# Performance work log

Measured on AMD Instinct MI355X. Metric: run time of the kernel, lower is better.

## Reference

```python
import jax, jax.numpy as jnp
import numpy as np
import math

DIM = 1024
N_HEADS = 16
HEAD_DIM = DIM // N_HEADS
MAX_SEQ_LEN = 2048


def rope_tables(seq_len, head_dim):
    inv_freq = 1.0 / (10000.0 ** (jnp.arange(0, head_dim, 2, dtype=jnp.float32) / head_dim))
    t = jnp.arange(seq_len, dtype=jnp.float32)
    freqs = jnp.einsum('i,j->ij', t, inv_freq)          # [T, D/2]
    emb = jnp.concatenate([freqs, freqs], axis=-1)      # [T, D]
    return jnp.cos(emb), jnp.sin(emb)


def rotate_half(x):
    x1, x2 = jnp.split(x, 2, axis=-1)
    return jnp.concatenate([-x2, x1], axis=-1)


def setup_inputs() -> dict:
    key = jax.random.key(0)
    k1, k2, k3 = jax.random.split(key, 3)
    B, T = 4, 2048
    x = jax.random.normal(k1, (B, T, DIM), dtype=jnp.float32)
    # Linear(dim, 3*dim, bias=False) and Linear(dim, dim, bias=False); stored as [in, out]
    Wqkv = jax.random.normal(k2, (DIM, 3 * DIM), dtype=jnp.float32) * (1.0 / math.sqrt(DIM))
    Wproj = jax.random.normal(k3, (DIM, DIM), dtype=jnp.float32) * (1.0 / math.sqrt(DIM))
    return {"x": x, "Wqkv": Wqkv, "Wproj": Wproj}


def reference(x, Wqkv, Wproj):
    B, T, C = x.shape
    qkv = x @ Wqkv                                       # [B,T,3C]
    q, k, v = jnp.split(qkv, 3, axis=-1)
    # [B,T,C] -> [B,H,T,D]
    def to_heads(t_):
        return t_.reshape(B, T, N_HEADS, HEAD_DIM).transpose(0, 2, 1, 3)
    q, k, v = to_heads(q), to_heads(k), to_heads(v)
    cos, sin = rope_tables(T, HEAD_DIM)                  # [T,D]
    cos = cos[None, None, :, :]
    sin = sin[None, None, :, :]
    q = q * cos + rotate_half(q) * sin
    k = k * cos + rotate_half(k) * sin
    scale = 1.0 / math.sqrt(HEAD_DIM)
    att = jnp.einsum('bhqd,bhkd->bhqk', q, k) * scale    # [B,H,T,T]
    causal = jnp.triu(jnp.ones((T, T), dtype=bool), k=1)
    att = jnp.where(causal[None, None], -jnp.inf, att)
    att = jax.nn.softmax(att, axis=-1)
    y = jnp.einsum('bhqk,bhkd->bhqd', att, v)            # [B,H,T,D]
    y = y.transpose(0, 2, 1, 3).reshape(B, T, C)
    return y @ Wproj
```

## Files before the change

### kernel.cpp

```cpp
#include <hip/hip_runtime.h>
#include <hip/hip_bf16.h>

typedef unsigned short u16;
typedef __attribute__((ext_vector_type(8))) short short8;
typedef __attribute__((ext_vector_type(4))) float floatx4;

__device__ __forceinline__ u16 f2bf(float f) {
    union { float f; unsigned u; } v; v.f = f;
    unsigned r = v.u + 0x7fffu + ((v.u >> 16) & 1u);
    return (u16)(r >> 16);
}
__device__ __forceinline__ float fexp2(float x) {
#if __has_builtin(__builtin_amdgcn_exp2f)
    return __builtin_amdgcn_exp2f(x);
#else
    return exp2f(x);
#endif
}
__device__ __forceinline__ unsigned cvtpk_bf16(float lo, float hi) {
    unsigned r;
    asm("v_cvt_pk_bf16_f32 %0, %1, %2" : "=v"(r) : "v"(lo), "v"(hi));
    return r;
}
__device__ __forceinline__ void permlane32_swap(unsigned &a, unsigned &b) {
    asm("v_permlane32_swap_b32 %0, %1" : "+v"(a), "+v"(b));
}
__device__ __forceinline__ void permlane16_swap(unsigned &a, unsigned &b) {
    asm("v_permlane16_swap_b32 %0, %1" : "+v"(a), "+v"(b));
}

__device__ __forceinline__ void async_load16(const void* g, void* l) {
    __builtin_amdgcn_global_load_lds(
        (const __attribute__((address_space(1))) unsigned int*)g,
        (__attribute__((address_space(3))) unsigned int*)l, 16, 0, 0);
}

#define B_   4
#define T_   2048
#define NH_  16
#define HD_  64
#define DIM_ 1024
#define M_   (B_ * T_)
#define NQKV (3 * DIM_)
#define NT_  16
#define LOG2E 1.4426950408889634f

__global__ void cvt_x(const float* __restrict__ in, u16* __restrict__ out) {
    int idx = blockIdx.x * 256 + threadIdx.x;
    float4 v = ((const float4*)in)[idx];
    ushort4 o;
    o.x = f2bf(v.x); o.y = f2bf(v.y); o.z = f2bf(v.z); o.w = f2bf(v.w);
    ((ushort4*)out)[idx] = o;
}

__global__ void transpose_cvt(const float* __restrict__ in, u16* __restrict__ out,
                              int R, int Cn) {
    __shared__ float tile[32][33];
    int c0 = blockIdx.x * 32, r0 = blockIdx.y * 32;
    int tx = threadIdx.x, ty = threadIdx.y;
#pragma unroll
    for (int i = 0; i < 4; ++i)
        tile[ty + i * 8][tx] = in[(size_t)(r0 + ty + i * 8) * Cn + c0 + tx];
    __syncthreads();
#pragma unroll
    for (int i = 0; i < 4; ++i)
        out[(size_t)(c0 + ty + i * 8) * R + r0 + tx] = f2bf(tile[tx][ty + i * 8]);
}

__global__ void rope_table(float* __restrict__ tabc, float* __restrict__ tabs) {
    int idx = blockIdx.x * 256 + threadIdx.x;
    if (idx >= T_ * 32) return;
    int t = idx >> 5, j = idx & 31;
    double invf = pow(10000.0, -(double)j / 32.0);
    double th = (double)t * invf;
    tabc[idx] = (float)cos(th);
    tabs[idx] = (float)sin(th);
}

__global__ void v_transpose(const u16* __restrict__ Vh, u16* __restrict__ Vt) {
    __shared__ u16 tile[64 * 68];
    const int tid = threadIdx.x;
    const int bh = blockIdx.y, b = bh >> 4, h = bh & 15;
    const int t0 = blockIdx.x * 64;
    {
        int lr = tid >> 2;
        int lc = tid & 3;
        const u16* src = Vh + ((size_t)(b * T_ + t0 + lr)) * DIM_ + h * HD_;
#pragma unroll
        for (int j = 0; j < 4; ++j) {
            int c = (lc + j * 4) * 4;
            *(uint2*)&tile[lr * 68 + c] = *(const uint2*)(src + c);
        }
    }
    __syncthreads();
    {
        int d2 = tid >> 3, tseg = tid & 7;
        u16 lo8[8], hi8[8];
#pragma unroll
        for (int j = 0; j < 8; ++j) {
            unsigned w = *(const unsigned*)&tile[(tseg * 8 + j) * 68 + d2 * 2];
            lo8[j] = (u16)(w & 0xffffu);
            hi8[j] = (u16)(w >> 16);
        }
        size_t ob = ((size_t)bh * HD_ + 2 * d2) * T_ + t0 + tseg * 8;
        *(uint4*)(Vt + ob) = *(const uint4*)lo8;
        *(uint4*)(Vt + ob + T_) = *(const uint4*)hi8;
    }
}

__device__ __forceinline__ void gemm_core(const u16* __restrict__ A,
                                          const u16* __restrict__ Bt,
                                          u16* smem, int m0, int n0, int tid,
                                          floatx4 (&acc)[4][4]) {
    const int wave = tid >> 6, lane = tid & 63;
    const int ln15 = lane & 15, quad = lane >> 4;
    const int wm = (wave & 1) * 64, wn = (wave >> 1) * 64;
    const int l8 = lane & 7, ld8 = lane >> 3;
    const int sgc = (l8 ^ ld8) * 8;
    const int K = DIM_;

    const u16* aS = A + (size_t)(m0 + wave * 16 + ld8) * K + sgc;
    const u16* bS = Bt + (size_t)(n0 + wave * 32 + ld8) * K + sgc;

    auto issueA_B0 = [&](int k2, u16* As2, u16* Bs2) {
        async_load16(aS + k2,          As2 + (wave * 16) * 64);
        async_load16(aS + 8 * K + k2,  As2 + (wave * 16 + 8) * 64);
        async_load16(bS + k2,          Bs2 + (wave * 32) * 64);
    };
    auto issueB123 = [&](int k2, u16* Bs2) {
        async_load16(bS + 8 * K + k2,  Bs2 + (wave * 32 + 8) * 64);
        async_load16(bS + 16 * K + k2, Bs2 + (wave * 32 + 16) * 64);
        async_load16(bS + 24 * K + k2, Bs2 + (wave * 32 + 24) * 64);
    };
    auto compute = [&](const u16* As_c, const u16* Bs_c, int c4) {
        short8 af[4], bfv[4];
#pragma unroll
        for (int i = 0; i < 4; ++i) {
            int row = wm + i * 16 + ln15;
            af[i] = *(const short8*)&As_c[row * 64 + (((c4 + quad) ^ (row & 7)) << 3)];
        }
#pragma unroll
        for (int j = 0; j < 4; ++j) {
            int row = wn + j * 16 + ln15;
            bfv[j] = *(const short8*)&Bs_c[row * 64 + (((c4 + quad) ^ (row & 7)) << 3)];
        }
        __builtin_amdgcn_s_setprio(1);
#pragma unroll
        for (int i = 0; i < 4; ++i)
#pragma unroll
            for (int j = 0; j < 4; ++j)
                acc[i][j] = __builtin_amdgcn_mfma_f32_16x16x32_bf16(
                    af[i], bfv[j], acc[i][j], 0, 0, 0);
        __builtin_amdgcn_s_setprio(0);
    };

    issueA_B0(0, smem, smem + 24576);
    issueB123(0, smem + 24576);
    issueA_B0(64, smem + 8192, smem + 24576 + 16384);
    issueB123(64, smem + 24576 + 16384);

#pragma unroll 1
    for (int t = 0; t < NT_; ++t) {
        if (t < NT_ - 1) asm volatile("s_waitcnt vmcnt(6)" ::: "memory");
        else             asm volatile("s_waitcnt vmcnt(0)" ::: "memory");
        __builtin_amdgcn_s_barrier();
        asm volatile("" ::: "memory");

        const int cb = t % 3, cb2 = (t + 2) % 3;
        const u16* As_c = smem + cb * 8192;
        const u16* Bs_c = smem + 24576 + cb * 16384;
        u16* As2 = smem + cb2 * 8192;
        u16* Bs2 = smem + 24576 + cb2 * 16384;
        const bool iss = t < NT_ - 2;
        const int k2 = (t + 2) * 64;

        if (iss) issueA_B0(k2, As2, Bs2);
        compute(As_c, Bs_c, 0);
        asm volatile("" ::: "memory");
        __builtin_amdgcn_s_barrier();
        asm volatile("" ::: "memory");

        if (iss) issueB123(k2, Bs2);
        compute(As_c, Bs_c, 4);
        asm volatile("" ::: "memory");
    }
}

__global__ __launch_bounds__(512, 2) void gemm_qkv(const u16* __restrict__ A,
                                                   const u16* __restrict__ Bt,
                                                   const float* __restrict__ tabc,
                                                   const float* __restrict__ tabs,
                                                   u16* __restrict__ Qo,
                                                   u16* __restrict__ Ko,
                                                   u16* __restrict__ Vh) {
    __shared__ __align__(16) u16 smem[73728];
    const int tid = threadIdx.x;
    const int bid = blockIdx.x;
    const int wg = (bid & 7) * 96 + (bid >> 3);
    const int bx = wg / 64, by = wg - bx * 64;
    const int m0 = by * 128, n0 = bx * 256;

    floatx4 acc[4][4] = {};
    gemm_core(A, Bt, smem, m0, n0, tid, acc);

    const int wave = tid >> 6, lane = tid & 63;
    const int ln15 = lane & 15, quad = lane >> 4;
    const int wm = (wave & 1) * 64, wn = (wave >> 1) * 64;

    __syncthreads();
    u16* Es = smem;
    const int sel = n0 >> 10;
    auto es_put = [&](int row, int col, u16 v) {
        int c = col >> 3;
        int pc = (c & 24) | ((c & 7) ^ (row & 7));
        Es[row * 256 + pc * 8 + (col & 7)] = v;
    };
    if (sel == 2) {
#pragma unroll
        for (int i = 0; i < 4; ++i)
#pragma unroll
            for (int j = 0; j < 4; ++j)
#pragma unroll
                for (int r = 0; r < 4; ++r)
                    es_put(wm + i * 16 + quad * 4 + r, wn + j * 16 + ln15,
                           f2bf(acc[i][j][r]));
    } else {
        const float scale = sel ? 1.0f : 0.125f * LOG2E;
#pragma unroll
        for (int i = 0; i < 4; ++i)
#pragma unroll
            for (int jjl = 0; jjl < 2; ++jjl) {
                int j = jjl * 16 + ln15;
#pragma unroll
                for (int r = 0; r < 4; ++r) {
                    int row = wm + i * 16 + quad * 4 + r;
                    int t = (m0 + row) & (T_ - 1);
                    float cs = tabc[t * 32 + j], sn = tabs[t * 32 + j];
                    float xl = acc[i][jjl][r], xh = acc[i][jjl + 2][r];
                    es_put(row, wn + j,      f2bf((xl * cs - xh * sn) * scale));
                    es_put(row, wn + j + 32, f2bf((xh * cs + xl * sn) * scale));
                }
            }
    }
    __syncthreads();
    const int bb = m0 >> 11;
    u16* outqk = (sel == 1) ? Ko : Qo;
#pragma unroll
    for (int k = 0; k < 8; ++k) {
        int cid = tid + k * 512;
        int row = cid >> 5, c = cid & 31;
        int pc = (c & 24) | ((c & 7) ^ (row & 7));
        uint4 v = *(const uint4*)&Es[row * 256 + pc * 8];
        if (sel == 2) {
            *(uint4*)&Vh[(size_t)(m0 + row) * DIM_ + (n0 & 1023) + c * 8] = v;
        } else {
            int h = ((n0 & 1023) >> 6) + (c >> 3);
            int d = (c & 7) * 8;
            int t = (m0 + row) & (T_ - 1);
            *(uint4*)&outqk[((size_t)(bb * NH_ + h) * T_ + t) * HD_ + d] = v;
        }
    }
}

__global__ __launch_bounds__(512, 2) void gemm_proj(const u16* __restrict__ A,
                                                    const u16* __restrict__ Bt,
                                                    float* __restrict__ C) {
    __shared__ __align__(16) u16 smem[73728];
    const int tid = threadIdx.x;
    const int bid = blockIdx.x;
    const int wg = (bid & 7) * 32 + (bid >> 3);
    const int bx = wg / 64, by = wg - bx * 64;
    const int m0 = by * 128, n0 = bx * 256;

    floatx4 acc[4][4] = {};
    gemm_core(A, Bt, smem, m0, n0, tid, acc);

    const int wave = tid >> 6, lane = tid & 63;
    const int ln15 = lane & 15, quad = lane >> 4;
    const int wm = (wave & 1) * 64, wn = (wave >> 1) * 64;
#pragma unroll
    for (int i = 0; i < 4; ++i)
#pragma unroll
        for (int j = 0; j < 4; ++j)
#pragma unroll
            for (int r = 0; r < 4; ++r) {
                int m = m0 + wm + i * 16 + quad * 4 + r;
                int n = n0 + wn + j * 16 + ln15;
                C[(size_t)m * DIM_ + n] = acc[i][j][r];
            }
}

__global__ __launch_bounds__(256, 5) void attn_kernel(const u16* __restrict__ Q,
                                                      const u16* __restrict__ Kh,
                                                      const u16* __restrict__ Vt,
                                                      u16* __restrict__ Y) {
    __shared__ __align__(16) u16 Kl[2][64 * 64];
    __shared__ __align__(16) u16 Vl[2][64 * 64];
    const int tid = threadIdx.x, wave = tid >> 6, lane = tid & 63;
    const int ln15 = lane & 15, quad = lane >> 4;
    const int bid = blockIdx.x;
    const int wg = (bid & 7) * 128 + (bid >> 3);
    const int p = wg & 15;
    const int bh = wg >> 4;
    const int b = bh >> 4, h = bh & 15;
    const int l8 = lane & 7, ld8 = lane >> 3;
    const int sgc = l8 ^ ld8;

    const u16* kbase = Kh + (size_t)bh * T_ * HD_;
    const u16* vbase = Vt + (size_t)bh * HD_ * T_;
    const short8 ones = {0x3F80, 0x3F80, 0x3F80, 0x3F80,
                         0x3F80, 0x3F80, 0x3F80, 0x3F80};
    const int srow = wave * 16;

#pragma unroll
    for (int half = 0; half < 2; ++half) {
        const int tidx = half ? p : (31 - p);
        const int q0 = tidx * 64;
        const int bm = q0 + srow;

        const u16* qp = Q + ((size_t)bh * T_ + bm + ln15) * HD_;
        short8 qf0 = *(const short8*)(qp + quad * 8);
        short8 qf1 = *(const short8*)(qp + 32 + quad * 8);

        floatx4 o[5] = {};

        __syncthreads();
#pragma unroll
        for (int it = 0; it < 2; ++it) {
            int r = srow + it * 8;
            async_load16(kbase + (size_t)(r + ld8) * HD_ + sgc * 8, &Kl[0][r * 64]);
            async_load16(vbase + (size_t)(r + ld8) * T_ + sgc * 8, &Vl[0][r * 64]);
        }

        for (int kt = 0; kt <= tidx; ++kt) {
            const int cur = kt & 1;
            __syncthreads();
            if (kt < tidx) {
                const int kn = (kt + 1) * 64;
#pragma unroll
                for (int it = 0; it < 2; ++it) {
                    int r = srow + it * 8;
                    async_load16(kbase + (size_t)(kn + r + ld8) * HD_ + sgc * 8,
                                 &Kl[cur ^ 1][r * 64]);
                    async_load16(vbase + (size_t)(r + ld8) * T_ + kn + sgc * 8,
                                 &Vl[cur ^ 1][r * 64]);
                }
            }
            floatx4 s[4] = {};
            __builtin_amdgcn_s_setprio(1);
#pragma unroll
            for (int nt = 0; nt < 4; ++nt) {
                int row = nt * 16 + ln15;
                short8 kf0 = *(const short8*)&Kl[cur][row * 64 + ((quad ^ (row & 7)) << 3)];
                short8 kf1 = *(const short8*)&Kl[cur][row * 64 + (((4 + quad) ^ (row & 7)) << 3)];
                s[nt] = __builtin_amdgcn_mfma_f32_16x16x32_bf16(kf0, qf0, s[nt], 0, 0, 0);
                s[nt] = __builtin_amdgcn_mfma_f32_16x16x32_bf16(kf1, qf1, s[nt], 0, 0, 0);
            }
            __builtin_amdgcn_s_setprio(0);
            if (kt == tidx) {
                const int lim = srow + ln15;
#pragma unroll
                for (int nt = 0; nt < 4; ++nt) {
                    int key = nt * 16 + quad * 4;
#pragma unroll
                    for (int r = 0; r < 4; ++r)
                        s[nt][r] = (key + r > lim) ? 0.f : fexp2(s[nt][r]);
                }
            } else {
#pragma unroll
                for (int nt = 0; nt < 4; ++nt)
#pragma unroll
                    for (int r = 0; r < 4; ++r) s[nt][r] = fexp2(s[nt][r]);
            }
            unsigned x0 = cvtpk_bf16(s[0][0], s[0][1]);
            unsigned x1 = cvtpk_bf16(s[1][0], s[1][1]);
            unsigned y0 = cvtpk_bf16(s[0][2], s[0][3]);
            unsigned y1 = cvtpk_bf16(s[1][2], s[1][3]);
            unsigned x2 = cvtpk_bf16(s[2][0], s[2][1]);
            unsigned x3 = cvtpk_bf16(s[3][0], s[3][1]);
            unsigned y2 = cvtpk_bf16(s[2][2], s[2][3]);
            unsigned y3 = cvtpk_bf16(s[3][2], s[3][3]);
            permlane32_swap(x0, x1); permlane16_swap(x0, x1);
            permlane32_swap(y0, y1); permlane16_swap(y0, y1);
            permlane32_swap(x2, x3); permlane16_swap(x2, x3);
            permlane32_swap(y2, y3); permlane16_swap(y2, y3);
            union { unsigned u[4]; short8 s8; } pk0, pk1;
            pk0.u[0] = x0; pk0.u[1] = y0; pk0.u[2] = x1; pk0.u[3] = y1;
            pk1.u[0] = x2; pk1.u[1] = y2; pk1.u[2] = x3; pk1.u[3] = y3;
            __builtin_amdgcn_s_setprio(1);
#pragma unroll
            for (int nt = 0; nt < 4; ++nt) {
                int row = nt * 16 + ln15;
                short8 vf0 = *(const short8*)&Vl[cur][row * 64 + ((quad ^ (row & 7)) << 3)];
                short8 vf1 = *(const short8*)&Vl[cur][row * 64 + (((4 + quad) ^ (row & 7)) << 3)];
                o[nt] = __builtin_amdgcn_mfma_f32_16x16x32_bf16(pk0.s8, vf0, o[nt], 0, 0, 0);
                o[nt] = __builtin_amdgcn_mfma_f32_16x16x32_bf16(pk1.s8, vf1, o[nt], 0, 0, 0);
            }
            o[4] = __builtin_amdgcn_mfma_f32_16x16x32_bf16(pk0.s8, ones, o[4], 0, 0, 0);
            o[4] = __builtin_amdgcn_mfma_f32_16x16x32_bf16(pk1.s8, ones, o[4], 0, 0, 0);
            __builtin_amdgcn_s_setprio(0);
        }
#pragma unroll
        for (int r = 0; r < 4; ++r) {
            float inv = 1.f / o[4][r];
            int row = bm + quad * 4 + r;
            u16* yp = Y + ((size_t)(b * T_ + row)) * DIM_ + h * HD_;
#pragma unroll
            for (int nt = 0; nt < 4; ++nt)
                yp[nt * 16 + ln15] = f2bf(o[nt][r] * inv);
        }
    }
}

extern "C" void kernel_launch(void* const* d_in, const int* in_sizes, int n_in,
                              void* d_out, int out_size, void* d_ws, size_t ws_size,
                              hipStream_t stream) {
    const float* x     = (const float*)d_in[0];
    const float* Wqkv  = (const float*)d_in[1];
    const float* Wproj = (const float*)d_in[2];
    float* out = (float*)d_out;
    char* ws = (char*)d_ws;

    const size_t SZ_XB  = (size_t)M_ * DIM_ * 2;
    const size_t SZ_WQT = (size_t)NQKV * DIM_ * 2;
    const size_t SZ_WPT = (size_t)DIM_ * DIM_ * 2;
    const size_t SZ_Q   = SZ_XB;
    const size_t SZ_TAB = (size_t)T_ * 32 * 4;

    u16*   xb   = (u16*)(ws);
    u16*   wqt  = (u16*)(ws + SZ_XB);
    u16*   wpt  = (u16*)(ws + SZ_XB + SZ_WQT);
    u16*   qb   = (u16*)(ws + SZ_XB + SZ_WQT + SZ_WPT);
    u16*   kb   = (u16*)(ws + SZ_XB + SZ_WQT + SZ_WPT + SZ_Q);
    u16*   vhb  = (u16*)(ws + SZ_XB + SZ_WQT + SZ_WPT + 2 * SZ_Q);
    u16*   vtb  = (u16*)(ws + SZ_XB + SZ_WQT + SZ_WPT + 3 * SZ_Q);
    float* tabc = (float*)(ws + SZ_XB + SZ_WQT + SZ_WPT + 4 * SZ_Q);
    float* tabs = (float*)(ws + SZ_XB + SZ_WQT + SZ_WPT + 4 * SZ_Q + SZ_TAB);
    u16*   yb   = xb;

    rope_table<<<(T_ * 32 + 255) / 256, 256, 0, stream>>>(tabc, tabs);
    cvt_x<<<(M_ * DIM_ / 4) / 256, 256, 0, stream>>>(x, xb);
    transpose_cvt<<<dim3(NQKV / 32, DIM_ / 32), dim3(32, 8), 0, stream>>>(Wqkv, wqt, DIM_, NQKV);
    transpose_cvt<<<dim3(DIM_ / 32, DIM_ / 32), dim3(32, 8), 0, stream>>>(Wproj, wpt, DIM_, DIM_);
    gemm_qkv<<<768, 512, 0, stream>>>(xb, wqt, tabc, tabs, qb, kb, vhb);
    v_transpose<<<dim3(T_ / 64, B_ * NH_), 256, 0, stream>>>(vhb, vtb);
    attn_kernel<<<1024, 256, 0, stream>>>(qb, kb, vtb, yb);
    gemm_proj<<<256, 512, 0, stream>>>(yb, wpt, out);
}
```

Before: 239.9 us.

## Merge preprocessing kernels, fuse V transpose into QKV GEMM, retile projection GEMM

Four preprocessing launches (x conversion, two weight transposes, RoPE table) become one block-indexed kernel, and the separate V transpose kernel is dropped: the QKV GEMM epilogue now writes V already transposed from shared memory. The projection GEMM moves from 256 blocks of 128x256 tiles with 512 threads to 512 blocks of 128x128 tiles with 256 threads and a simpler double-buffered core. The intent is to cut launch overhead and an extra V round trip through memory, and to fill more CUs in the projection. The transposed V stores use scattered 2-byte LDS gathers and a different store pattern, which may cost epilogue time.

```diff
diff --git a/kernel.cpp b/kernel.cpp
--- a/kernel.cpp
+++ b/kernel.cpp
@@ -45,66 +45,43 @@
 #define NT_  16
 #define LOG2E 1.4426950408889634f
 
-__global__ void cvt_x(const float* __restrict__ in, u16* __restrict__ out) {
-    int idx = blockIdx.x * 256 + threadIdx.x;
-    float4 v = ((const float4*)in)[idx];
-    ushort4 o;
-    o.x = f2bf(v.x); o.y = f2bf(v.y); o.z = f2bf(v.z); o.w = f2bf(v.w);
-    ((ushort4*)out)[idx] = o;
-}
-
-__global__ void transpose_cvt(const float* __restrict__ in, u16* __restrict__ out,
-                              int R, int Cn) {
+__global__ __launch_bounds__(256) void preproc(const float* __restrict__ x,
+                                               const float* __restrict__ Wqkv,
+                                               const float* __restrict__ Wproj,
+                                               u16* __restrict__ xb,
+                                               u16* __restrict__ wqt,
+                                               u16* __restrict__ wpt,
+                                               float* __restrict__ tabc,
+                                               float* __restrict__ tabs) {
     __shared__ float tile[32][33];
-    int c0 = blockIdx.x * 32, r0 = blockIdx.y * 32;
-    int tx = threadIdx.x, ty = threadIdx.y;
-#pragma unroll
-    for (int i = 0; i < 4; ++i)
-        tile[ty + i * 8][tx] = in[(size_t)(r0 + ty + i * 8) * Cn + c0 + tx];
-    __syncthreads();
-#pragma unroll
-    for (int i = 0; i < 4; ++i)
-        out[(size_t)(c0 + ty + i * 8) * R + r0 + tx] = f2bf(tile[tx][ty + i * 8]);
-}
-
-__global__ void rope_table(float* __restrict__ tabc, float* __restrict__ tabs) {
-    int idx = blockIdx.x * 256 + threadIdx.x;
-    if (idx >= T_ * 32) return;
-    int t = idx >> 5, j = idx & 31;
-    double invf = pow(10000.0, -(double)j / 32.0);
-    double th = (double)t * invf;
-    tabc[idx] = (float)cos(th);
-    tabs[idx] = (float)sin(th);
-}
-
-__global__ void v_transpose(const u16* __restrict__ Vh, u16* __restrict__ Vt) {
-    __shared__ u16 tile[64 * 68];
-    const int tid = threadIdx.x;
-    const int bh = blockIdx.y, b = bh >> 4, h = bh & 15;
-    const int t0 = blockIdx.x * 64;
-    {
-        int lr = tid >> 2;
-        int lc = tid & 3;
-        const u16* src = Vh + ((size_t)(b * T_ + t0 + lr)) * DIM_ + h * HD_;
-#pragma unroll
-        for (int j = 0; j < 4; ++j) {
-            int c = (lc + j * 4) * 4;
-            *(uint2*)&tile[lr * 68 + c] = *(const uint2*)(src + c);
-        }
-    }
-    __syncthreads();
-    {
-        int d2 = tid >> 3, tseg = tid & 7;
-        u16 lo8[8], hi8[8];
-#pragma unroll
-        for (int j = 0; j < 8; ++j) {
-            unsigned w = *(const unsigned*)&tile[(tseg * 8 + j) * 68 + d2 * 2];
-            lo8[j] = (u16)(w & 0xffffu);
-            hi8[j] = (u16)(w >> 16);
-        }
-        size_t ob = ((size_t)bh * HD_ + 2 * d2) * T_ + t0 + tseg * 8;
-        *(uint4*)(Vt + ob) = *(const uint4*)lo8;
-        *(uint4*)(Vt + ob + T_) = *(const uint4*)hi8;
+    const int bid = blockIdx.x, tid = threadIdx.x;
+    if (bid < 8192) {
+        int idx = bid * 256 + tid;
+        float4 v = ((const float4*)x)[idx];
+        ushort4 o;
+        o.x = f2bf(v.x); o.y = f2bf(v.y); o.z = f2bf(v.z); o.w = f2bf(v.w);
+        ((ushort4*)xb)[idx] = o;
+    } else if (bid < 12288) {
+        const float* in; u16* outp; int Cn, bx, by;
+        if (bid < 11264) { int blk = bid - 8192;  in = Wqkv;  outp = wqt; Cn = NQKV; bx = blk % 96; by = blk / 96; }
+        else             { int blk = bid - 11264; in = Wproj; outp = wpt; Cn = DIM_; bx = blk & 31; by = blk >> 5; }
+        const int R = DIM_;
+        int c0 = bx * 32, r0 = by * 32;
+        int tx = tid & 31, ty = tid >> 5;
+#pragma unroll
+        for (int i = 0; i < 4; ++i)
+            tile[ty + i * 8][tx] = in[(size_t)(r0 + ty + i * 8) * Cn + c0 + tx];
+        __syncthreads();
+#pragma unroll
+        for (int i = 0; i < 4; ++i)
+            outp[(size_t)(c0 + ty + i * 8) * R + r0 + tx] = f2bf(tile[tx][ty + i * 8]);
+    } else {
+        int idx = (bid - 12288) * 256 + tid;
+        int t = idx >> 5, j = idx & 31;
+        double invf = pow(10000.0, -(double)j / 32.0);
+        double th = (double)t * invf;
+        tabc[idx] = (float)cos(th);
+        tabs[idx] = (float)sin(th);
     }
 }
 
@@ -192,7 +169,7 @@
                                                    const float* __restrict__ tabs,
                                                    u16* __restrict__ Qo,
                                                    u16* __restrict__ Ko,
-                                                   u16* __restrict__ Vh) {
+                                                   u16* __restrict__ Vt) {
     __shared__ __align__(16) u16 smem[73728];
     const int tid = threadIdx.x;
     const int bid = blockIdx.x;
@@ -243,17 +220,41 @@
             }
     }
     __syncthreads();
-    const int bb = m0 >> 11;
-    u16* outqk = (sel == 1) ? Ko : Qo;
-#pragma unroll
-    for (int k = 0; k < 8; ++k) {
-        int cid = tid + k * 512;
-        int row = cid >> 5, c = cid & 31;
-        int pc = (c & 24) | ((c & 7) ^ (row & 7));
-        uint4 v = *(const uint4*)&Es[row * 256 + pc * 8];
-        if (sel == 2) {
-            *(uint4*)&Vh[(size_t)(m0 + row) * DIM_ + (n0 & 1023) + c * 8] = v;
-        } else {
+    if (sel == 2) {
+        const int bq = m0 >> 11;
+        const int t0 = m0 & (T_ - 1);
+        const int h0 = (n0 & 1023) >> 6;
+#pragma unroll
+        for (int a = 0; a < 4; ++a) {
+            int aid = tid + a * 512;
+            int hh = aid >> 9;
+            int rem = aid & 511;
+            int tseg = rem >> 5;
+            int d2 = rem & 31;
+            int col = hh * 64 + 2 * d2;
+            int cch = col >> 3;
+            u16 lo8[8], hi8[8];
+#pragma unroll
+            for (int j = 0; j < 8; ++j) {
+                int row = tseg * 8 + j;
+                int pc = (cch & 24) | ((cch & 7) ^ (row & 7));
+                unsigned w = *(const unsigned*)&Es[row * 256 + pc * 8 + (col & 7)];
+                lo8[j] = (u16)(w & 0xffffu);
+                hi8[j] = (u16)(w >> 16);
+            }
+            size_t ob = ((size_t)((bq * NH_ + h0 + hh) * HD_) + 2 * d2) * T_ + t0 + tseg * 8;
+            *(uint4*)(Vt + ob) = *(const uint4*)lo8;
+            *(uint4*)(Vt + ob + T_) = *(const uint4*)hi8;
+        }
+    } else {
+        const int bb = m0 >> 11;
+        u16* outqk = (sel == 1) ? Ko : Qo;
+#pragma unroll
+        for (int k = 0; k < 8; ++k) {
+            int cid = tid + k * 512;
+            int row = cid >> 5, c = cid & 31;
+            int pc = (c & 24) | ((c & 7) ^ (row & 7));
+            uint4 v = *(const uint4*)&Es[row * 256 + pc * 8];
             int h = ((n0 & 1023) >> 6) + (c >> 3);
             int d = (c & 7) * 8;
             int t = (m0 + row) & (T_ - 1);
@@ -262,31 +263,91 @@
     }
 }
 
-__global__ __launch_bounds__(512, 2) void gemm_proj(const u16* __restrict__ A,
-                                                    const u16* __restrict__ Bt,
-                                                    float* __restrict__ C) {
-    __shared__ __align__(16) u16 smem[73728];
-    const int tid = threadIdx.x;
-    const int bid = blockIdx.x;
-    const int wg = (bid & 7) * 32 + (bid >> 3);
-    const int bx = wg / 64, by = wg - bx * 64;
-    const int m0 = by * 128, n0 = bx * 256;
-
-    floatx4 acc[4][4] = {};
-    gemm_core(A, Bt, smem, m0, n0, tid, acc);
-
+__device__ __forceinline__ void gemm_core128(const u16* __restrict__ A,
+                                             const u16* __restrict__ Bt,
+                                             u16* smem, int m0, int n0, int tid,
+                                             floatx4 (&acc)[4][4]) {
     const int wave = tid >> 6, lane = tid & 63;
     const int ln15 = lane & 15, quad = lane >> 4;
     const int wm = (wave & 1) * 64, wn = (wave >> 1) * 64;
+    const int l8 = lane & 7, ld8 = lane >> 3;
+    const int sgc = (l8 ^ ld8) * 8;
+    const int K = DIM_;
+
+    const u16* aS = A + (size_t)(m0 + wave * 32 + ld8) * K + sgc;
+    const u16* bS = Bt + (size_t)(n0 + wave * 32 + ld8) * K + sgc;
+
+    auto stage = [&](int k0, u16* buf) {
+#pragma unroll
+        for (int it = 0; it < 4; ++it) {
+            async_load16(aS + (size_t)(it * 8) * K + k0,
+                         buf + (wave * 32 + it * 8) * 64);
+            async_load16(bS + (size_t)(it * 8) * K + k0,
+                         buf + 8192 + (wave * 32 + it * 8) * 64);
+        }
+    };
+    auto compute = [&](const u16* buf, int c4) {
+        short8 af[4], bfv[4];
+#pragma unroll
+        for (int i = 0; i < 4; ++i) {
+            int row = wm + i * 16 + ln15;
+            af[i] = *(const short8*)&buf[row * 64 + (((c4 + quad) ^ (row & 7)) << 3)];
+        }
+#pragma unroll
+        for (int j = 0; j < 4; ++j) {
+            int row = wn + j * 16 + ln15;
+            bfv[j] = *(const short8*)&buf[8192 + row * 64 + (((c4 + quad) ^ (row & 7)) << 3)];
+        }
+        __builtin_amdgcn_s_setprio(1);
+#pragma unroll
+        for (int i = 0; i < 4; ++i)
+#pragma unroll
+            for (int j = 0; j < 4; ++j)
+                acc[i][j] = __builtin_amdgcn_mfma_f32_16x16x32_bf16(
+                    af[i], bfv[j], acc[i][j], 0, 0, 0);
+        __builtin_amdgcn_s_setprio(0);
+    };
+
+    stage(0, smem);
+#pragma unroll 1
+    for (int t = 0; t < NT_; ++t) {
+        asm volatile("s_waitcnt vmcnt(0)" ::: "memory");
+        __builtin_amdgcn_s_barrier();
+        asm volatile("" ::: "memory");
+        if (t + 1 < NT_) stage((t + 1) * 64, smem + ((t + 1) & 1) * 16384);
+        const u16* cur = smem + (t & 1) * 16384;
+        compute(cur, 0);
+        compute(cur, 4);
+        asm volatile("" ::: "memory");
+    }
+}
+
+__global__ __launch_bounds__(256, 4) void gemm_proj(const u16* __restrict__ A,
+                                                    const u16* __restrict__ Bt,
+                                                    float* __restrict__ C) {
+    __shared__ __align__(16) u16 smem[32768];
+    const int tid = threadIdx.x;
+    const int bid = blockIdx.x;
+    const int local = bid >> 3;
+    const int by = (bid & 7) * 8 + (local & 7);
+    const int bx = local >> 3;
+    const int m0 = by * 128, n0 = bx * 128;
+
+    floatx4 acc[4][4] = {};
+    gemm_core128(A, Bt, smem, m0, n0, tid, acc);
+
+    const int wave = tid >> 6, lane = tid & 63;
+    const int ln15 = lane & 15, quad = lane >> 4;
+    const int wm = (wave & 1) * 64, wn = (wave >> 1) * 64;
 #pragma unroll
     for (int i = 0; i < 4; ++i)
 #pragma unroll
-        for (int j = 0; j < 4; ++j)
+        for (int jj = 0; jj < 4; ++jj)
 #pragma unroll
             for (int r = 0; r < 4; ++r) {
                 int m = m0 + wm + i * 16 + quad * 4 + r;
-                int n = n0 + wn + j * 16 + ln15;
-                C[(size_t)m * DIM_ + n] = acc[i][j][r];
+                int n = n0 + wn + jj * 16 + ln15;
+                C[(size_t)m * DIM_ + n] = acc[i][jj][r];
             }
 }
 
@@ -432,18 +493,13 @@
     u16*   wpt  = (u16*)(ws + SZ_XB + SZ_WQT);
     u16*   qb   = (u16*)(ws + SZ_XB + SZ_WQT + SZ_WPT);
     u16*   kb   = (u16*)(ws + SZ_XB + SZ_WQT + SZ_WPT + SZ_Q);
-    u16*   vhb  = (u16*)(ws + SZ_XB + SZ_WQT + SZ_WPT + 2 * SZ_Q);
     u16*   vtb  = (u16*)(ws + SZ_XB + SZ_WQT + SZ_WPT + 3 * SZ_Q);
     float* tabc = (float*)(ws + SZ_XB + SZ_WQT + SZ_WPT + 4 * SZ_Q);
     float* tabs = (float*)(ws + SZ_XB + SZ_WQT + SZ_WPT + 4 * SZ_Q + SZ_TAB);
     u16*   yb   = xb;
 
-    rope_table<<<(T_ * 32 + 255) / 256, 256, 0, stream>>>(tabc, tabs);
-    cvt_x<<<(M_ * DIM_ / 4) / 256, 256, 0, stream>>>(x, xb);
-    transpose_cvt<<<dim3(NQKV / 32, DIM_ / 32), dim3(32, 8), 0, stream>>>(Wqkv, wqt, DIM_, NQKV);
-    transpose_cvt<<<dim3(DIM_ / 32, DIM_ / 32), dim3(32, 8), 0, stream>>>(Wproj, wpt, DIM_, DIM_);
-    gemm_qkv<<<768, 512, 0, stream>>>(xb, wqt, tabc, tabs, qb, kb, vhb);
-    v_transpose<<<dim3(T_ / 64, B_ * NH_), 256, 0, stream>>>(vhb, vtb);
+    preproc<<<12544, 256, 0, stream>>>(x, Wqkv, Wproj, xb, wqt, wpt, tabc, tabs);
+    gemm_qkv<<<768, 512, 0, stream>>>(xb, wqt, tabc, tabs, qb, kb, vtb);
     attn_kernel<<<1024, 256, 0, stream>>>(qb, kb, vtb, yb);
-    gemm_proj<<<256, 512, 0, stream>>>(yb, wpt, out);
-}
+    gemm_proj<<<512, 256, 0, stream>>>(yb, wpt, out);
+}
```

Result: faster. 232.7 us (-3.0%).
